# Kernel tuning notes

Measured on AMD Instinct MI355X. Metric: run time of the kernel, lower is better.

## Reference

```python
import jax, jax.numpy as jnp
import numpy as np

H, DH, M, ITERS = 8, 64, 256, 6   # heads, dim_head, num_landmarks, pinv iters
DIM = H * DH                      # 512
KERNEL = 33                       # residual depthwise conv kernel


def setup_inputs() -> dict:
    key = jax.random.key(0)
    ks = jax.random.split(key, 5)
    b, n = 2, 8192                # n multiple of M -> no divisibility padding
    x = jax.random.normal(ks[0], (b, n, DIM), jnp.float32)
    ln_gamma = jnp.ones((DIM,), jnp.float32)
    ln_beta = jnp.zeros((DIM,), jnp.float32)
    w_qkv = jax.random.normal(ks[1], (DIM, 3 * DIM), jnp.float32) * 0.02
    w_out = jax.random.normal(ks[2], (DIM, DIM), jnp.float32) * 0.02
    b_out = jnp.zeros((DIM,), jnp.float32)
    res_kernel = jax.random.normal(ks[3], (H, 1, KERNEL, 1), jnp.float32) * 0.02
    return {"x": x, "ln_gamma": ln_gamma, "ln_beta": ln_beta, "w_qkv": w_qkv,
            "w_out": w_out, "b_out": b_out, "res_kernel": res_kernel}


def _pinv(a, iters):
    # lucidrains moore_penrose_iter_pinv (Newton-Schulz iteration)
    abs_a = jnp.abs(a)
    scale = abs_a.sum(-1).max() * abs_a.sum(-2).max()
    z = jnp.swapaxes(a, -1, -2) / scale
    I = jnp.eye(a.shape[-1], dtype=a.dtype)
    for _ in range(iters):
        az = a @ z
        z = 0.25 * z @ (13.0 * I - az @ (15.0 * I - az @ (7.0 * I - az)))
    return z


def reference(x, ln_gamma, ln_beta, w_qkv, w_out, b_out, res_kernel):
    b, n, d = x.shape
    # pre-LayerNorm (eps 1e-5)
    mu = jnp.mean(x, -1, keepdims=True)
    var = jnp.var(x, -1, keepdims=True)
    xn = (x - mu) * jax.lax.rsqrt(var + 1e-5) * ln_gamma + ln_beta
    # qkv projection (bias-free)
    q, k, v = jnp.split(xn @ w_qkv, 3, axis=-1)
    to_heads = lambda t: t.reshape(b, n, H, DH).transpose(0, 2, 1, 3)  # b h n d
    q, k, v = to_heads(q), to_heads(k), to_heads(v)
    q = q * (DH ** -0.5)
    # landmarks: mean over groups of l consecutive tokens ('(m l) d -> m d')
    l = n // M
    q_l = q.reshape(b, H, M, l, DH).mean(3)  # b h M d
    k_l = k.reshape(b, H, M, l, DH).mean(3)
    sim1 = jnp.einsum('bhnd,bhmd->bhnm', q, k_l)      # queries vs k-landmarks
    sim2 = jnp.einsum('bhid,bhjd->bhij', q_l, k_l)    # landmarks vs landmarks
    sim3 = jnp.einsum('bhmd,bhnd->bhmn', q_l, k)      # q-landmarks vs keys
    a1 = jax.nn.softmax(sim1, axis=-1)
    a2 = jax.nn.softmax(sim2, axis=-1)
    a3 = jax.nn.softmax(sim3, axis=-1)
    a2_inv = _pinv(a2, ITERS)
    out = (a1 @ a2_inv) @ (a3 @ v)  # b h n d
    # residual depthwise conv over the sequence axis (Conv2d kernel (33,1), groups=H)
    pad = KERNEL // 2
    out = out + jax.lax.conv_general_dilated(
        v, res_kernel, (1, 1), [(pad, pad), (0, 0)],
        dimension_numbers=('NCHW', 'OIHW', 'NCHW'), feature_group_count=H)
    out = out.transpose(0, 2, 1, 3).reshape(b, n, d)
    out = out @ w_out + b_out  # to_out Linear (dropout inactive at eval)
    return x + out             # TransLayer residual
```

## Files before the change

kernel.cpp:

```cpp
#include <hip/hip_runtime.h>
#include <math.h>

#define H_ 8
#define DH_ 64
#define DIM_ 512
#define M_ 256
#define N_ 8192
#define BH_ 16
#define LG_ 32
#define KC_ 33
#define CH_ 16
#define NTI_ 8

typedef __attribute__((ext_vector_type(8))) short bf16x8;
typedef __attribute__((ext_vector_type(4))) short s16x4;
typedef __attribute__((ext_vector_type(4))) float f32x4;

__device__ __forceinline__ short f2bf(float f) {
  unsigned u = __float_as_uint(f);
  unsigned r = (u + 0x7FFF + ((u >> 16) & 1)) >> 16;
  return (short)r;
}
__device__ __forceinline__ float bf2f(short s) {
  return __uint_as_float(((unsigned)(unsigned short)s) << 16);
}

__device__ __forceinline__ void mfma_nt_core(const short* __restrict__ A,
                                             const short* __restrict__ Bt, int K,
                                             int m0, int n0, size_t lda, size_t ldb,
                                             f32x4 acc[4][4], short* As, short* Bs) {
  const int tid = threadIdx.x;
  const int wave = tid >> 6, lane = tid & 63;
  const int wr = (wave >> 1) * 64, wc = (wave & 1) * 64;
  const int mi = lane & 15, quad = lane >> 4;
  for (int k0 = 0; k0 < K; k0 += 32) {
#pragma unroll
    for (int t = 0; t < 2; ++t) {
      const int cbase = (t * 4 + wave) * 64;
      const int chunk = cbase + lane;
      const int row = chunk >> 2, cc = (chunk & 3) * 8;
      __builtin_amdgcn_global_load_lds(
          (const __attribute__((address_space(1))) void*)(A + (size_t)(m0 + row) * lda + k0 + cc),
          (__attribute__((address_space(3))) void*)(As + (size_t)cbase * 8), 16, 0, 0);
      __builtin_amdgcn_global_load_lds(
          (const __attribute__((address_space(1))) void*)(Bt + (size_t)(n0 + row) * ldb + k0 + cc),
          (__attribute__((address_space(3))) void*)(Bs + (size_t)cbase * 8), 16, 0, 0);
    }
    __syncthreads();
    bf16x8 af[4], bf[4];
#pragma unroll
    for (int i = 0; i < 4; ++i)
      af[i] = *(const bf16x8*)&As[(wr + i * 16 + mi) * 32 + quad * 8];
#pragma unroll
    for (int j = 0; j < 4; ++j)
      bf[j] = *(const bf16x8*)&Bs[(wc + j * 16 + mi) * 32 + quad * 8];
#pragma unroll
    for (int i = 0; i < 4; ++i)
#pragma unroll
      for (int j = 0; j < 4; ++j)
        acc[i][j] = __builtin_amdgcn_mfma_f32_16x16x32_bf16(af[i], bf[j], acc[i][j], 0, 0, 0);
    __syncthreads();
  }
}

__device__ __forceinline__ void xcd_remap128(int& bx, int& by) {
  const int lin = blockIdx.y * 128 + blockIdx.x;
  const int cpx = (gridDim.y * 128) >> 3;
  const int sw = (lin & 7) * cpx + (lin >> 3);
  bx = sw & 127;
  by = sw >> 7;
}

__global__ __launch_bounds__(256) void qkv_mfma(const short* __restrict__ xnb,
                                                const short* __restrict__ wt,
                                                short* __restrict__ qb, short* __restrict__ kb,
                                                short* __restrict__ vb) {
  __shared__ short As[128 * 32], Bs[128 * 32];
  f32x4 acc[4][4] = {};
  int bx, by;
  xcd_remap128(bx, by);
  const int m0 = bx * 128, n0 = by * 128;
  mfma_nt_core(xnb, wt, DIM_, m0, n0, DIM_, DIM_, acc, As, Bs);
  const int wave = threadIdx.x >> 6, lane = threadIdx.x & 63;
  const int wr = (wave >> 1) * 64, wc = (wave & 1) * 64;
  const int mi = lane & 15, quad = lane >> 4;
  const int which = n0 >> 9;
  short* dst = which == 0 ? qb : which == 1 ? kb : vb;
  const float sc = which == 0 ? 0.125f : 1.0f;
#pragma unroll
  for (int j = 0; j < 4; ++j) {
    const int col = n0 + wc + j * 16 + mi;
    const int h = (col >> 6) & 7, d = col & 63;
#pragma unroll
    for (int i = 0; i < 4; ++i) {
#pragma unroll
      for (int r = 0; r < 4; ++r) {
        const int row = m0 + wr + i * 16 + quad * 4 + r;
        const int b = row >> 13, t = row & (N_ - 1);
        dst[((size_t)(b * H_ + h) * N_ + t) * DH_ + d] = f2bf(acc[i][j][r] * sc);
      }
    }
  }
}

__global__ __launch_bounds__(256) void final_mfma(const short* __restrict__ omb,
                                                  const short* __restrict__ wt,
                                                  const float* __restrict__ x,
                                                  const float* __restrict__ bout,
                                                  float* __restrict__ y) {
  __shared__ short As[128 * 32], Bs[128 * 32];
  f32x4 acc[4][4] = {};
  int bx, by;
  xcd_remap128(bx, by);
  const int m0 = bx * 128, n0 = by * 128;
  mfma_nt_core(omb, wt, DIM_, m0, n0, DIM_, DIM_, acc, As, Bs);
  const int wave = threadIdx.x >> 6, lane = threadIdx.x & 63;
  const int wr = (wave >> 1) * 64, wc = (wave & 1) * 64;
  const int mi = lane & 15, quad = lane >> 4;
#pragma unroll
  for (int j = 0; j < 4; ++j) {
    const int col = n0 + wc + j * 16 + mi;
    const float bo = bout[col];
#pragma unroll
    for (int i = 0; i < 4; ++i) {
#pragma unroll
      for (int r = 0; r < 4; ++r) {
        const int row = m0 + wr + i * 16 + quad * 4 + r;
        y[(size_t)row * DIM_ + col] = acc[i][j][r] + x[(size_t)row * DIM_ + col] + bo;
      }
    }
  }
}

__global__ __launch_bounds__(256) void convt_kernel(const float* __restrict__ in,
                                                    short* __restrict__ out, int K, int N) {
  __shared__ float tile[32][33];
  const int n0 = blockIdx.x * 32, k0 = blockIdx.y * 32;
  const int tx = threadIdx.x & 31, ty = threadIdx.x >> 5;
  for (int r = ty; r < 32; r += 8) tile[r][tx] = in[(size_t)(k0 + r) * N + n0 + tx];
  __syncthreads();
  for (int r = ty; r < 32; r += 8) out[(size_t)(n0 + r) * K + k0 + tx] = f2bf(tile[tx][r]);
}

__global__ __launch_bounds__(256) void vt_kernel(const short* __restrict__ vb,
                                                 short* __restrict__ vtb) {
  __shared__ short tile[32][33];
  const int t0 = blockIdx.x * 32, d0 = blockIdx.y * 32, bh = blockIdx.z;
  const int tx = threadIdx.x & 31, ty = threadIdx.x >> 5;
  for (int r = ty; r < 32; r += 8)
    tile[r][tx] = vb[((size_t)bh * N_ + t0 + r) * DH_ + d0 + tx];
  __syncthreads();
  for (int r = ty; r < 32; r += 8)
    vtb[((size_t)bh * DH_ + d0 + r) * N_ + t0 + tx] = tile[tx][r];
}

__global__ __launch_bounds__(256) void ln_kernel(const float* __restrict__ x,
                                                 const float* __restrict__ gamma,
                                                 const float* __restrict__ beta,
                                                 short* __restrict__ xnb) {
  const int row = blockIdx.x * 4 + (threadIdx.x >> 6);
  const int lane = threadIdx.x & 63;
  const float4* xr = (const float4*)(x + (size_t)row * DIM_) + lane * 2;
  const float4 v0 = xr[0], v1 = xr[1];
  float s = v0.x + v0.y + v0.z + v0.w + v1.x + v1.y + v1.z + v1.w;
  float ss = v0.x * v0.x + v0.y * v0.y + v0.z * v0.z + v0.w * v0.w +
             v1.x * v1.x + v1.y * v1.y + v1.z * v1.z + v1.w * v1.w;
#pragma unroll
  for (int off = 1; off < 64; off <<= 1) {
    s += __shfl_xor(s, off, 64);
    ss += __shfl_xor(ss, off, 64);
  }
  const float mu = s * (1.0f / DIM_);
  const float var = ss * (1.0f / DIM_) - mu * mu;
  const float rs = rsqrtf(var + 1e-5f);
  const float4 g0 = ((const float4*)gamma)[lane * 2], g1 = ((const float4*)gamma)[lane * 2 + 1];
  const float4 b0 = ((const float4*)beta)[lane * 2], b1 = ((const float4*)beta)[lane * 2 + 1];
  bf16x8 o;
  o[0] = f2bf((v0.x - mu) * rs * g0.x + b0.x);
  o[1] = f2bf((v0.y - mu) * rs * g0.y + b0.y);
  o[2] = f2bf((v0.z - mu) * rs * g0.z + b0.z);
  o[3] = f2bf((v0.w - mu) * rs * g0.w + b0.w);
  o[4] = f2bf((v1.x - mu) * rs * g1.x + b1.x);
  o[5] = f2bf((v1.y - mu) * rs * g1.y + b1.y);
  o[6] = f2bf((v1.z - mu) * rs * g1.z + b1.z);
  o[7] = f2bf((v1.w - mu) * rs * g1.w + b1.w);
  *(bf16x8*)(xnb + (size_t)row * DIM_ + lane * 8) = o;
}

__global__ __launch_bounds__(256) void landmark_kernel(const short* __restrict__ qb,
                                                       const short* __restrict__ kb,
                                                       float* __restrict__ ql,
                                                       float* __restrict__ kl,
                                                       short* __restrict__ qlb,
                                                       short* __restrict__ klb) {
  const int idx = blockIdx.x * 256 + threadIdx.x;
  const int d = idx & (DH_ - 1);
  const int m = (idx >> 6) & (M_ - 1);
  const int bh = idx >> 14;
  const size_t base = ((size_t)bh * N_ + m * LG_) * DH_ + d;
  float sq = 0.f, sk = 0.f;
#pragma unroll 8
  for (int t = 0; t < LG_; ++t) {
    sq += bf2f(qb[base + (size_t)t * DH_]);
    sk += bf2f(kb[base + (size_t)t * DH_]);
  }
  sq *= (1.0f / LG_);
  sk *= (1.0f / LG_);
  ql[idx] = sq;
  kl[idx] = sk;
  qlb[idx] = f2bf(sq);
  klb[idx] = f2bf(sk);
}

__global__ __launch_bounds__(256) void sim2_softmax(const float* __restrict__ ql,
                                                    const float* __restrict__ kl,
                                                    float* __restrict__ a2,
                                                    short* __restrict__ a2b) {
  const int i = blockIdx.x, bh = blockIdx.y, j = threadIdx.x;
  __shared__ float qrow[DH_];
  if (j < DH_) qrow[j] = ql[((size_t)bh * M_ + i) * DH_ + j];
  __syncthreads();
  const float* kr = kl + ((size_t)bh * M_ + j) * DH_;
  float s = 0.f;
#pragma unroll 16
  for (int d = 0; d < DH_; ++d) s += qrow[d] * kr[d];
  __shared__ float red[256];
  red[j] = s;
  __syncthreads();
  for (int off = 128; off > 0; off >>= 1) {
    if (j < off) red[j] = fmaxf(red[j], red[j + off]);
    __syncthreads();
  }
  const float mx = red[0];
  __syncthreads();
  const float e = expf(s - mx);
  red[j] = e;
  __syncthreads();
  for (int off = 128; off > 0; off >>= 1) {
    if (j < off) red[j] += red[j + off];
    __syncthreads();
  }
  const float out = e / red[0];
  a2[((size_t)bh * M_ + i) * M_ + j] = out;
  a2b[((size_t)bh * M_ + i) * M_ + j] = f2bf(out);
}

__global__ __launch_bounds__(256) void colmax_kernel(const float* __restrict__ a2,
                                                     unsigned int* __restrict__ scalebits) {
  const int bh = blockIdx.x, j = threadIdx.x;
  const float* mat = a2 + (size_t)bh * M_ * M_;
  float s = 0.f;
  for (int i = 0; i < M_; ++i) s += fabsf(mat[i * M_ + j]);
  __shared__ float red[256];
  red[j] = s;
  __syncthreads();
  for (int off = 128; off > 0; off >>= 1) {
    if (j < off) red[j] = fmaxf(red[j], red[j + off]);
    __syncthreads();
  }
  if (j == 0) atomicMax(scalebits, __float_as_uint(red[0]));
}

__global__ __launch_bounds__(256) void transpose_scale(const float* __restrict__ a2,
                                                       short* __restrict__ z0b,
                                                       const unsigned int* __restrict__ scalebits) {
  const float inv = 1.0f / __uint_as_float(*scalebits);
  const int idx = blockIdx.x * 256 + threadIdx.x;
  const int j = idx & (M_ - 1), i = (idx >> 8) & (M_ - 1), bh = idx >> 16;
  z0b[idx] = f2bf(a2[((size_t)bh * M_ + j) * M_ + i] * inv);
}

__device__ __forceinline__ void ns_core(const short* __restrict__ A, const short* __restrict__ B,
                                        int m0, int n0, short* Bs, f32x4 acc[4]) {
  const int tid = threadIdx.x, wave = tid >> 6, lane = tid & 63;
  const int mi = lane & 15, quad = lane >> 4;
  const int bkk = tid & 31, g = tid >> 5;
  bf16x8 bv[8];
#pragma unroll
  for (int kc = 0; kc < 8; ++kc)
    bv[kc] = *(const bf16x8*)(B + (size_t)(kc * 32 + bkk) * M_ + n0 + g * 8);
  const short* arow = A + (size_t)(m0 + wave * 16 + mi) * M_;
  bf16x8 af[8];
#pragma unroll
  for (int k0 = 0; k0 < 8; ++k0)
    af[k0] = *(const bf16x8*)(arow + k0 * 32 + quad * 8);
#pragma unroll
  for (int kc = 0; kc < 8; ++kc)
#pragma unroll
    for (int e = 0; e < 8; ++e)
      Bs[(g * 8 + e) * 260 + kc * 32 + bkk] = bv[kc][e];
  __syncthreads();
#pragma unroll
  for (int k0 = 0; k0 < 8; ++k0) {
#pragma unroll
    for (int j = 0; j < 4; ++j) {
      union { bf16x8 v; s16x4 h[2]; } bfr;
      const short* bp = &Bs[(j * 16 + mi) * 260 + k0 * 32 + quad * 8];
      bfr.h[0] = *(const s16x4*)bp;
      bfr.h[1] = *(const s16x4*)(bp + 4);
      acc[j] = __builtin_amdgcn_mfma_f32_16x16x32_bf16(af[k0], bfr.v, acc[j], 0, 0, 0);
    }
  }
}

__device__ __forceinline__ int ns_remap() {
  const int lin = blockIdx.y * 16 + blockIdx.x;
  return (lin & 7) * (gridDim.y << 1) + (lin >> 3);
}

__global__ __launch_bounds__(256) void ns_gemm0(const short* __restrict__ A,
                                                const short* __restrict__ B,
                                                short* __restrict__ C) {
  __shared__ short Bs[64 * 260];
  const int id = ns_remap();
  const int bx = id & 15, by = id >> 4;
  const int m0 = (bx >> 2) * 64, n0 = (bx & 3) * 64;
  const size_t mo = (size_t)by * (M_ * M_);
  f32x4 acc[4] = {};
  ns_core(A + mo, B + mo, m0, n0, Bs, acc);
  const int wave = threadIdx.x >> 6, lane = threadIdx.x & 63;
  const int mi = lane & 15, quad = lane >> 4;
#pragma unroll
  for (int j = 0; j < 4; ++j)
#pragma unroll
    for (int r = 0; r < 4; ++r) {
      const int row = m0 + wave * 16 + quad * 4 + r, col = n0 + j * 16 + mi;
      C[mo + (size_t)row * M_ + col] = f2bf(acc[j][r]);
    }
}

__global__ __launch_bounds__(256) void ns_stageA(const short* __restrict__ z,
                                                 const short* __restrict__ y,
                                                 short* __restrict__ p1,
                                                 short* __restrict__ y2,
                                                 short* __restrict__ w) {
  __shared__ short Bs[64 * 260];
  const int id = ns_remap();
  const int bx = id & 15, by = id >> 4;
  const int m0 = (bx >> 2) * 64, n0 = (bx & 3) * 64;
  const int sel = by & 1;
  const size_t mo = (size_t)(by >> 1) * (M_ * M_);
  f32x4 acc[4] = {};
  ns_core((sel ? y : z) + mo, y + mo, m0, n0, Bs, acc);
  const int wave = threadIdx.x >> 6, lane = threadIdx.x & 63;
  const int mi = lane & 15, quad = lane >> 4;
#pragma unroll
  for (int j = 0; j < 4; ++j)
#pragma unroll
    for (int r = 0; r < 4; ++r) {
      const int row = m0 + wave * 16 + quad * 4 + r, col = n0 + j * 16 + mi;
      const size_t idx = mo + (size_t)row * M_ + col;
      if (sel) {
        y2[idx] = f2bf(acc[j][r]);
        w[idx] = f2bf(1.75f * bf2f(y[idx]) - 0.25f * acc[j][r]);
      } else {
        p1[idx] = f2bf(acc[j][r]);
      }
    }
}

__global__ __launch_bounds__(256) void ns_stageB(const short* __restrict__ p1,
                                                 const short* __restrict__ y2,
                                                 const short* __restrict__ w,
                                                 const short* __restrict__ z,
                                                 const short* __restrict__ y,
                                                 short* __restrict__ zo,
                                                 short* __restrict__ yo,
                                                 float* __restrict__ zf, int zonly) {
  __shared__ short Bs[64 * 260];
  const int id = ns_remap();
  const int bx = id & 15, by = id >> 4;
  const int m0 = (bx >> 2) * 64, n0 = (bx & 3) * 64;
  const int sel = zonly ? 0 : (by & 1);
  const size_t mo = (size_t)(zonly ? by : (by >> 1)) * (M_ * M_);
  f32x4 acc[4] = {};
  ns_core((sel ? y2 : p1) + mo, w + mo, m0, n0, Bs, acc);
  const int wave = threadIdx.x >> 6, lane = threadIdx.x & 63;
  const int mi = lane & 15, quad = lane >> 4;
#pragma unroll
  for (int j = 0; j < 4; ++j)
#pragma unroll
    for (int r = 0; r < 4; ++r) {
      const int row = m0 + wave * 16 + quad * 4 + r, col = n0 + j * 16 + mi;
      const size_t idx = mo + (size_t)row * M_ + col;
      if (sel) {
        yo[idx] = f2bf(3.25f * bf2f(y[idx]) - 3.75f * bf2f(y2[idx]) + acc[j][r]);
      } else {
        const float v = 3.25f * bf2f(z[idx]) - 3.75f * bf2f(p1[idx]) + acc[j][r];
        zo[idx] = f2bf(v);
        if (zf) zf[idx] = v;
      }
    }
}

__device__ __forceinline__ void mm_step(float (*As)[68], float (*Bs)[68],
                                        int tr, int tc, float acc[4][4]) {
#pragma unroll
  for (int kk = 0; kk < 16; ++kk) {
    const float4 a4 = *(const float4*)&As[kk][tr * 4];
    const float4 b4 = *(const float4*)&Bs[kk][tc * 4];
    const float a[4] = {a4.x, a4.y, a4.z, a4.w};
    const float b[4] = {b4.x, b4.y, b4.z, b4.w};
#pragma unroll
    for (int i = 0; i < 4; ++i)
#pragma unroll
      for (int j = 0; j < 4; ++j) acc[i][j] = fmaf(a[i], b[j], acc[i][j]);
  }
}

__device__ __forceinline__ void load_a_tile(const float* A, int lda, int m0, int k0,
                                            int tid, float (*As)[68]) {
  const int r = tid >> 2, kq = tid & 3;
  const float4 a4 = *(const float4*)(A + (size_t)(m0 + r) * lda + k0 + kq * 4);
  As[kq * 4 + 0][r] = a4.x;
  As[kq * 4 + 1][r] = a4.y;
  As[kq * 4 + 2][r] = a4.z;
  As[kq * 4 + 3][r] = a4.w;
}

__device__ __forceinline__ void load_b_nn(const float* B, int ldb, int k0, int n0,
                                          int tid, float (*Bs)[68]) {
  const int kr = tid >> 4, c4 = tid & 15;
  const float4 b4 = *(const float4*)(B + (size_t)(k0 + kr) * ldb + n0 + c4 * 4);
  *(float4*)&Bs[kr][c4 * 4] = b4;
}

__global__ __launch_bounds__(256) void gemm_nn64(const float* __restrict__ A, int lda,
                                                 long long strideA,
                                                 const float* __restrict__ B, long long strideB,
                                                 float* __restrict__ C, long long strideC,
                                                 int kchunk) {
  const int bz = blockIdx.z;
  A += (size_t)bz * strideA;
  B += (size_t)bz * strideB;
  C += (size_t)bz * strideC;
  const int m0 = blockIdx.x * 64;
  const int tid = threadIdx.x, tr = tid >> 4, tc = tid & 15;
  __shared__ float As[16][68], Bs[16][68];
  float acc[4][4] = {};
  for (int k0 = 0; k0 < kchunk; k0 += 16) {
    load_a_tile(A, lda, m0, k0, tid, As);
    load_b_nn(B, DH_, k0, 0, tid, Bs);
    __syncthreads();
    mm_step(As, Bs, tr, tc, acc);
    __syncthreads();
  }
#pragma unroll
  for (int i = 0; i < 4; ++i) {
    const int row = m0 + tr * 4 + i;
    *(float4*)(C + (size_t)row * DH_ + tc * 4) =
        make_float4(acc[i][0], acc[i][1], acc[i][2], acc[i][3]);
  }
}

__device__ __forceinline__ void stage_ks(const short* __restrict__ kb, int bh, int n0,
                                         int wave, int lane, short* ks) {
#pragma unroll
  for (int i = 0; i < 2; ++i) {
    const int cb = i * 256 + wave * 64;
    const int c = cb + lane;
    const int row = c >> 3, cc = c & 7;
    __builtin_amdgcn_global_load_lds(
        (const __attribute__((address_space(1))) void*)(
            kb + ((size_t)bh * N_ + n0 + row) * DH_ + ((cc ^ (row & 7)) * 8)),
        (__attribute__((address_space(3))) void*)(ks + (size_t)cb * 8), 16, 0, 0);
  }
}

__device__ __forceinline__ void stage_vs(const short* __restrict__ vtb, int bh, int n0,
                                         int wave, int lane, short* vs) {
#pragma unroll
  for (int i = 0; i < 2; ++i) {
    const int cb = i * 256 + wave * 64;
    const int c = cb + lane;
    const int row = c >> 3, cc = c & 7;
    __builtin_amdgcn_global_load_lds(
        (const __attribute__((address_space(1))) void*)(
            vtb + ((size_t)bh * DH_ + row) * N_ + n0 + ((cc ^ (row & 7)) * 8)),
        (__attribute__((address_space(3))) void*)(vs + (size_t)cb * 8), 16, 0, 0);
  }
}

__global__ __launch_bounds__(256) void a3_flash(const short* __restrict__ qlb,
                                                const short* __restrict__ kb,
                                                const short* __restrict__ vtb,
                                                float* __restrict__ Opart,
                                                float* __restrict__ mpart,
                                                float* __restrict__ lpart) {
  const int chunk = blockIdx.x, rt = blockIdx.y, bh = blockIdx.z;
  __shared__ short ks[2][64 * 64];
  __shared__ short vs[2][64 * 64];
  __shared__ short ps[64 * 64];
  const int tid = threadIdx.x, wave = tid >> 6, lane = tid & 63;
  const int mi = lane & 15, quad = lane >> 4;
  const short* qrow = qlb + ((size_t)bh * M_ + rt * 64 + wave * 16 + mi) * DH_;
  const bf16x8 aq0 = *(const bf16x8*)(qrow + quad * 8);
  const bf16x8 aq1 = *(const bf16x8*)(qrow + 32 + quad * 8);
  float m[4] = {-INFINITY, -INFINITY, -INFINITY, -INFINITY};
  float l[4] = {0.f, 0.f, 0.f, 0.f};
  f32x4 o[4] = {};
  const int nbase = chunk * (N_ / CH_);
  stage_ks(kb, bh, nbase, wave, lane, ks[0]);
  stage_vs(vtb, bh, nbase, wave, lane, vs[0]);
  __syncthreads();
  for (int t = 0; t < NTI_; ++t) {
    const int cur = t & 1;
    if (t + 1 < NTI_) {
      stage_ks(kb, bh, nbase + (t + 1) * 64, wave, lane, ks[cur ^ 1]);
      stage_vs(vtb, bh, nbase + (t + 1) * 64, wave, lane, vs[cur ^ 1]);
    }
    f32x4 s[4];
#pragma unroll
    for (int j = 0; j < 4; ++j) {
      const int row = j * 16 + mi;
      const bf16x8 b0 = *(const bf16x8*)&ks[cur][row * 64 + ((quad ^ (row & 7)) * 8)];
      const bf16x8 b1 = *(const bf16x8*)&ks[cur][row * 64 + (((quad + 4) ^ (row & 7)) * 8)];
      f32x4 z = {0.f, 0.f, 0.f, 0.f};
      z = __builtin_amdgcn_mfma_f32_16x16x32_bf16(aq0, b0, z, 0, 0, 0);
      s[j] = __builtin_amdgcn_mfma_f32_16x16x32_bf16(aq1, b1, z, 0, 0, 0);
    }
    float alpha[4];
#pragma unroll
    for (int r = 0; r < 4; ++r) {
      float v = fmaxf(fmaxf(s[0][r], s[1][r]), fmaxf(s[2][r], s[3][r]));
      v = fmaxf(v, __shfl_xor(v, 1, 64));
      v = fmaxf(v, __shfl_xor(v, 2, 64));
      v = fmaxf(v, __shfl_xor(v, 4, 64));
      v = fmaxf(v, __shfl_xor(v, 8, 64));
      const float mnew = fmaxf(m[r], v);
      alpha[r] = __expf(m[r] - mnew);
      m[r] = mnew;
    }
    float rs[4] = {0.f, 0.f, 0.f, 0.f};
#pragma unroll
    for (int j = 0; j < 4; ++j)
#pragma unroll
      for (int r = 0; r < 4; ++r) {
        const float p = __expf(s[j][r] - m[r]);
        rs[r] += p;
        const int prow = wave * 16 + quad * 4 + r;
        const int pcol = j * 16 + mi;
        ps[prow * 64 + (((pcol >> 3) ^ (prow & 7)) * 8) + (pcol & 7)] = f2bf(p);
      }
#pragma unroll
    for (int r = 0; r < 4; ++r) {
      l[r] = l[r] * alpha[r] + rs[r];
#pragma unroll
      for (int j = 0; j < 4; ++j) o[j][r] *= alpha[r];
    }
    const int prow = wave * 16 + mi;
    const bf16x8 ap0 = *(const bf16x8*)&ps[prow * 64 + ((quad ^ (mi & 7)) * 8)];
    const bf16x8 ap1 = *(const bf16x8*)&ps[prow * 64 + (((quad + 4) ^ (mi & 7)) * 8)];
#pragma unroll
    for (int j = 0; j < 4; ++j) {
      const int vrow = j * 16 + mi;
      const bf16x8 b0 = *(const bf16x8*)&vs[cur][vrow * 64 + ((quad ^ (vrow & 7)) * 8)];
      const bf16x8 b1 = *(const bf16x8*)&vs[cur][vrow * 64 + (((quad + 4) ^ (vrow & 7)) * 8)];
      o[j] = __builtin_amdgcn_mfma_f32_16x16x32_bf16(ap0, b0, o[j], 0, 0, 0);
      o[j] = __builtin_amdgcn_mfma_f32_16x16x32_bf16(ap1, b1, o[j], 0, 0, 0);
    }
    __syncthreads();
  }
#pragma unroll
  for (int r = 0; r < 4; ++r) {
    float v = l[r];
    v += __shfl_xor(v, 1, 64);
    v += __shfl_xor(v, 2, 64);
    v += __shfl_xor(v, 4, 64);
    v += __shfl_xor(v, 8, 64);
    l[r] = v;
  }
  const int p2 = bh * 4 + rt;
  float* Ob = Opart + ((size_t)chunk * 64 + p2) * 4096;
#pragma unroll
  for (int j = 0; j < 4; ++j)
#pragma unroll
    for (int r = 0; r < 4; ++r)
      Ob[(wave * 16 + quad * 4 + r) * 64 + j * 16 + mi] = o[j][r];
  if (mi == 0) {
#pragma unroll
    for (int r = 0; r < 4; ++r) {
      mpart[((size_t)chunk * 64 + p2) * 64 + wave * 16 + quad * 4 + r] = m[r];
      lpart[((size_t)chunk * 64 + p2) * 64 + wave * 16 + quad * 4 + r] = l[r];
    }
  }
}

__global__ __launch_bounds__(256) void a3_combine(const float* __restrict__ Opart,
                                                  const float* __restrict__ mpart,
                                                  const float* __restrict__ lpart,
                                                  float* __restrict__ a3v) {
  const int p2 = blockIdx.x, ds = blockIdx.y;
  const int bh = p2 >> 2, rt = p2 & 3;
  __shared__ float wgt[CH_][64];
  const int tid = threadIdx.x;
  if (tid < 64) {
    float mg = -INFINITY;
#pragma unroll
    for (int c = 0; c < CH_; ++c) mg = fmaxf(mg, mpart[((size_t)c * 64 + p2) * 64 + tid]);
    float e[CH_], lg = 0.f;
#pragma unroll
    for (int c = 0; c < CH_; ++c) {
      e[c] = __expf(mpart[((size_t)c * 64 + p2) * 64 + tid] - mg);
      lg += lpart[((size_t)c * 64 + p2) * 64 + tid] * e[c];
    }
    const float inv = 1.f / lg;
#pragma unroll
    for (int c = 0; c < CH_; ++c) wgt[c][tid] = e[c] * inv;
  }
  __syncthreads();
  for (int i = ds * 1024 + tid; i < ds * 1024 + 1024; i += 256) {
    const int row = i >> 6, d = i & 63;
    float s = 0.f;
#pragma unroll
    for (int c = 0; c < CH_; ++c) s += Opart[((size_t)c * 64 + p2) * 4096 + i] * wgt[c][row];
    a3v[((size_t)bh * M_ + rt * 64 + row) * DH_ + d] = s;
  }
}

__global__ __launch_bounds__(256) void w2t_kernel(const float* __restrict__ w2,
                                                  short* __restrict__ w2tb) {
  const int bh = blockIdx.x, tid = threadIdx.x;
  for (int i = tid; i < M_ * DH_; i += 256) {
    const int r = i >> 6, d = i & 63;
    w2tb[((size_t)bh * DH_ + d) * M_ + r] = f2bf(w2[(size_t)bh * M_ * DH_ + i]);
  }
}

__global__ __launch_bounds__(256, 4) void a1_conv(const short* __restrict__ qb,
                                                  const short* __restrict__ klb,
                                                  const short* __restrict__ w2tb,
                                                  const short* __restrict__ vtb,
                                                  const float* __restrict__ rk,
                                                  short* __restrict__ omb) {
  __shared__ __align__(16) char smem[34944];
  short* kls = (short*)smem;
  short* ps = (short*)smem;
  short* vwin = (short*)(smem + 17920);
  short* band = (short*)(smem + 32768);
  const int bh = blockIdx.y, t0 = blockIdx.x * 64;
  const int b = bh >> 3, h = bh & 7;
  const int tid = threadIdx.x, wave = tid >> 6, lane = tid & 63;
  const int mi = lane & 15, quad = lane >> 4;

  const short* qrow = qb + ((size_t)bh * N_ + t0 + wave * 16 + mi) * DH_;
  const bf16x8 aq0 = *(const bf16x8*)(qrow + quad * 8);
  const bf16x8 aq1 = *(const bf16x8*)(qrow + 32 + quad * 8);

  const int vd = tid & 63, cg0 = tid >> 6;
  bf16x8 vreg[4];
  {
    const short* vrow = vtb + ((size_t)bh * DH_ + vd) * N_;
#pragma unroll
    for (int slot = 0; slot < 4; ++slot) {
      const int ch = cg0 + slot * 4;
      bf16x8 vv = {};
      if (ch < 14) {
        const int tbase = t0 - 16 + ch * 8;
        if (tbase >= 0 && tbase + 8 <= N_) {
          vv = *(const bf16x8*)(vrow + tbase);
        } else {
#pragma unroll
          for (int e = 0; e < 8; ++e) {
            const int tt = tbase + e;
            vv[e] = (tt >= 0 && tt < N_) ? vrow[tt] : (short)0;
          }
        }
      }
      vreg[slot] = vv;
    }
  }
#pragma unroll
  for (int i = 0; i < 4; ++i) {
    const int idx = tid + i * 256;
    const int r = idx >> 6, c = idx & 63, u = c - r;
    band[r * 68 + c] = (u >= 0 && u < KC_) ? f2bf(rk[h * KC_ + u]) : (short)0;
  }

#pragma unroll
  for (int i = 0; i < 8; ++i) {
    const int cb = i * 256 + wave * 64;
    const int c = cb + lane;
    const int row = c >> 3, cc = c & 7;
    __builtin_amdgcn_global_load_lds(
        (const __attribute__((address_space(1))) void*)(
            klb + ((size_t)bh * M_ + row) * DH_ + (cc ^ (row & 7)) * 8),
        (__attribute__((address_space(3))) void*)(kls + (size_t)cb * 8), 16, 0, 0);
  }
  __syncthreads();

  f32x4 s[16] = {};
#pragma unroll
  for (int f = 0; f < 16; ++f) {
    const int row = f * 16 + mi;
    const bf16x8 blo = *(const bf16x8*)&kls[row * 64 + ((quad ^ (row & 7)) * 8)];
    const bf16x8 bhi = *(const bf16x8*)&kls[row * 64 + (((quad + 4) ^ (row & 7)) * 8)];
    f32x4 z = __builtin_amdgcn_mfma_f32_16x16x32_bf16(aq0, blo, s[f], 0, 0, 0);
    s[f] = __builtin_amdgcn_mfma_f32_16x16x32_bf16(aq1, bhi, z, 0, 0, 0);
  }
  float lsum[4];
#pragma unroll
  for (int r = 0; r < 4; ++r) {
    float v = s[0][r];
#pragma unroll
    for (int f = 1; f < 16; ++f) v = fmaxf(v, s[f][r]);
    v = fmaxf(v, __shfl_xor(v, 1, 64));
    v = fmaxf(v, __shfl_xor(v, 2, 64));
    v = fmaxf(v, __shfl_xor(v, 4, 64));
    v = fmaxf(v, __shfl_xor(v, 8, 64));
    float sum = 0.f;
#pragma unroll
    for (int f = 0; f < 16; ++f) {
      const float p = __expf(s[f][r] - v);
      s[f][r] = p;
      sum += p;
    }
    lsum[r] = sum;
  }
  __syncthreads();

#pragma unroll
  for (int slot = 0; slot < 4; ++slot) {
    const int ch = cg0 + slot * 4;
    if (ch < 14) *(bf16x8*)&vwin[vd * 116 + ch * 8] = vreg[slot];
  }

  f32x4 o[4] = {};
#pragma unroll
  for (int half = 0; half < 2; ++half) {
#pragma unroll
    for (int f = 0; f < 8; ++f)
#pragma unroll
      for (int r = 0; r < 4; ++r)
        ps[(wave * 16 + quad * 4 + r) * 140 + f * 16 + mi] = f2bf(s[half * 8 + f][r]);
#pragma unroll
    for (int k0 = 0; k0 < 4; ++k0) {
      union { bf16x8 v; s16x4 hh[2]; } ap;
      const short* pp = &ps[(wave * 16 + mi) * 140 + k0 * 32 + quad * 8];
      ap.hh[0] = *(const s16x4*)pp;
      ap.hh[1] = *(const s16x4*)(pp + 4);
#pragma unroll
      for (int j = 0; j < 4; ++j) {
        const bf16x8 bw = *(const bf16x8*)(w2tb + ((size_t)bh * DH_ + j * 16 + mi) * M_ +
                                           (half * 4 + k0) * 32 + quad * 8);
        o[j] = __builtin_amdgcn_mfma_f32_16x16x32_bf16(ap.v, bw, o[j], 0, 0, 0);
      }
    }
  }
#pragma unroll
  for (int r = 0; r < 4; ++r) {
    float v = lsum[r];
    v += __shfl_xor(v, 1, 64);
    v += __shfl_xor(v, 2, 64);
    v += __shfl_xor(v, 4, 64);
    v += __shfl_xor(v, 8, 64);
    const float inv = 1.f / v;
#pragma unroll
    for (int j = 0; j < 4; ++j) o[j][r] *= inv;
  }
  __syncthreads();

#pragma unroll
  for (int ks = 0; ks < 2; ++ks) {
    union { bf16x8 v; s16x4 hh[2]; } ab;
    const short* bp = &band[mi * 68 + ks * 32 + quad * 8];
    ab.hh[0] = *(const s16x4*)bp;
    ab.hh[1] = *(const s16x4*)(bp + 4);
#pragma unroll
    for (int j = 0; j < 4; ++j) {
      union { bf16x8 v; s16x4 hh[2]; } bv;
      const short* vp = &vwin[(j * 16 + mi) * 116 + wave * 16 + ks * 32 + quad * 8];
      bv.hh[0] = *(const s16x4*)vp;
      bv.hh[1] = *(const s16x4*)(vp + 4);
      o[j] = __builtin_amdgcn_mfma_f32_16x16x32_bf16(ab.v, bv.v, o[j], 0, 0, 0);
    }
  }
#pragma unroll
  for (int j = 0; j < 4; ++j) {
    const int d = j * 16 + mi;
#pragma unroll
    for (int r = 0; r < 4; ++r) {
      const int t = t0 + wave * 16 + quad * 4 + r;
      omb[((size_t)(b * N_ + t)) * DIM_ + h * DH_ + d] = f2bf(o[j][r]);
    }
  }
}

extern "C" void kernel_launch(void* const* d_in, const int* in_sizes, int n_in,
                              void* d_out, int out_size, void* d_ws, size_t ws_size,
                              hipStream_t stream) {
  (void)in_sizes; (void)n_in; (void)out_size;
  const float* x = (const float*)d_in[0];
  const float* gamma = (const float*)d_in[1];
  const float* beta = (const float*)d_in[2];
  const float* wqkv = (const float*)d_in[3];
  const float* wout = (const float*)d_in[4];
  const float* bout = (const float*)d_in[5];
  const float* rk = (const float*)d_in[6];
  float* y = (float*)d_out;
  float* ws = (float*)d_ws;

  size_t o = 0;
  short* xnb = (short*)(ws + o);   o += (size_t)2 * N_ * DIM_ / 2;
  short* wqkvt = (short*)(ws + o); o += (size_t)3 * DIM_ * DIM_ / 2;
  short* woutt = (short*)(ws + o); o += (size_t)DIM_ * DIM_ / 2;
  short* qb = (short*)(ws + o);    o += (size_t)BH_ * N_ * DH_ / 2;
  short* kb = (short*)(ws + o);    o += (size_t)BH_ * N_ * DH_ / 2;
  short* vb = (short*)(ws + o);    o += (size_t)BH_ * N_ * DH_ / 2;
  short* vtb = (short*)(ws + o);   o += (size_t)BH_ * N_ * DH_ / 2;
  float* ql = ws + o;  o += (size_t)BH_ * M_ * DH_;
  float* kl = ws + o;  o += (size_t)BH_ * M_ * DH_;
  short* qlb = (short*)(ws + o); o += (size_t)BH_ * M_ * DH_ / 2;
  short* klb = (short*)(ws + o); o += (size_t)BH_ * M_ * DH_ / 2;
  float* a2 = ws + o;  o += (size_t)BH_ * M_ * M_;
  float* z0f = ws + o; o += (size_t)BH_ * M_ * M_;
  short* a2b = (short*)(ws + o); o += (size_t)BH_ * M_ * M_ / 2;
  short* zb0 = (short*)(ws + o); o += (size_t)BH_ * M_ * M_ / 2;
  short* zb1 = (short*)(ws + o); o += (size_t)BH_ * M_ * M_ / 2;
  short* yb0 = (short*)(ws + o); o += (size_t)BH_ * M_ * M_ / 2;
  short* yb1 = (short*)(ws + o); o += (size_t)BH_ * M_ * M_ / 2;
  short* p1b = (short*)(ws + o); o += (size_t)BH_ * M_ * M_ / 2;
  short* y2b = (short*)(ws + o); o += (size_t)BH_ * M_ * M_ / 2;
  short* wb  = (short*)(ws + o); o += (size_t)BH_ * M_ * M_ / 2;
  float* Opart = ws + o; o += (size_t)CH_ * 64 * 4096;
  float* mpart = ws + o; o += (size_t)CH_ * 64 * 64;
  float* lpart = ws + o; o += (size_t)CH_ * 64 * 64;
  float* a3v = ws + o; o += (size_t)BH_ * M_ * DH_;
  float* w2 = ws + o;  o += (size_t)BH_ * M_ * DH_;
  short* w2tb = (short*)(ws + o); o += (size_t)BH_ * M_ * DH_ / 2;
  short* omb = (short*)(ws + o);  o += (size_t)2 * N_ * DIM_ / 2;
  unsigned int* scalebits = (unsigned int*)(ws + o); o += 16;
  if (ws_size < o * sizeof(float)) return;

  (void)hipMemsetAsync(scalebits, 0, 64, stream);
  ln_kernel<<<2 * N_ / 4, 256, 0, stream>>>(x, gamma, beta, xnb);
  convt_kernel<<<dim3(3 * DIM_ / 32, DIM_ / 32), 256, 0, stream>>>(wqkv, wqkvt, DIM_, 3 * DIM_);
  convt_kernel<<<dim3(DIM_ / 32, DIM_ / 32), 256, 0, stream>>>(wout, woutt, DIM_, DIM_);
  qkv_mfma<<<dim3(2 * N_ / 128, 3 * DIM_ / 128), 256, 0, stream>>>(xnb, wqkvt, qb, kb, vb);
  vt_kernel<<<dim3(N_ / 32, 2, BH_), 256, 0, stream>>>(vb, vtb);

  landmark_kernel<<<BH_ * M_ * DH_ / 256, 256, 0, stream>>>(qb, kb, ql, kl, qlb, klb);
  sim2_softmax<<<dim3(M_, BH_), 256, 0, stream>>>(ql, kl, a2, a2b);
  colmax_kernel<<<BH_, 256, 0, stream>>>(a2, scalebits);
  transpose_scale<<<BH_ * M_ * M_ / 256, 256, 0, stream>>>(a2, zb0, scalebits);

  a3_flash<<<dim3(CH_, 4, BH_), 256, 0, stream>>>(qlb, kb, vtb, Opart, mpart, lpart);
  a3_combine<<<dim3(64, 4), 256, 0, stream>>>(Opart, mpart, lpart, a3v);

  ns_gemm0<<<dim3(16, BH_), 256, 0, stream>>>(a2b, zb0, yb0);
  short* zc = zb0; short* zn = zb1; short* yc = yb0; short* yn = yb1;
  for (int it = 0; it < 6; ++it) {
    const int last = (it == 5);
    ns_stageA<<<dim3(16, 2 * BH_), 256, 0, stream>>>(zc, yc, p1b, y2b, wb);
    ns_stageB<<<dim3(16, last ? BH_ : 2 * BH_), 256, 0, stream>>>(
        p1b, y2b, wb, zc, yc, zn, yn, last ? z0f : nullptr, last);
    short* t;
    t = zc; zc = zn; zn = t;
    t = yc; yc = yn; yn = t;
  }

  gemm_nn64<<<dim3(M_ / 64, 1, BH_), 256, 0, stream>>>(
      z0f, M_, (long long)M_ * M_, a3v, (long long)M_ * DH_, w2, (long long)M_ * DH_, M_);
  w2t_kernel<<<BH_, 256, 0, stream>>>(w2, w2tb);

  a1_conv<<<dim3(N_ / 64, BH_), 256, 0, stream>>>(qb, klb, w2tb, vtb, rk, omb);

  final_mfma<<<dim3(2 * N_ / 128, DIM_ / 128), 256, 0, stream>>>(omb, woutt, x, bout, y);
}
```

Measured before the change: 453.8 us.

## Fuse Newton-Schulz pinv iterations into one cooperative kernel with grid syncs

Replaces the 13 separate Newton-Schulz GEMM launches with a single cooperative kernel of 512 blocks that uses grid.sync between stages, which removes per-launch overhead and the gaps between launches. It also fuses the bf16 transpose of w2 into the gemm_nn64 epilogue, so the w2t_kernel launch and the fp32 w2 buffer are no longer needed. The XCD block remapping is dropped from the qkv and final GEMMs. Grid-wide barriers add their own sync cost, need all 512 blocks to be co-resident, and the new transposed stores in gemm_nn64 are strided.

New measurement: 1.764 ms. +288.8%, slower.

```diff
diff --git a/kernel.cpp b/kernel.cpp
--- a/kernel.cpp
+++ b/kernel.cpp
@@ -1,5 +1,8 @@
 #include <hip/hip_runtime.h>
+#include <hip/hip_cooperative_groups.h>
 #include <math.h>
+
+namespace cg = cooperative_groups;
 
 #define H_ 8
 #define DH_ 64
@@ -63,23 +66,13 @@
   }
 }
 
-__device__ __forceinline__ void xcd_remap128(int& bx, int& by) {
-  const int lin = blockIdx.y * 128 + blockIdx.x;
-  const int cpx = (gridDim.y * 128) >> 3;
-  const int sw = (lin & 7) * cpx + (lin >> 3);
-  bx = sw & 127;
-  by = sw >> 7;
-}
-
 __global__ __launch_bounds__(256) void qkv_mfma(const short* __restrict__ xnb,
                                                 const short* __restrict__ wt,
                                                 short* __restrict__ qb, short* __restrict__ kb,
                                                 short* __restrict__ vb) {
   __shared__ short As[128 * 32], Bs[128 * 32];
   f32x4 acc[4][4] = {};
-  int bx, by;
-  xcd_remap128(bx, by);
-  const int m0 = bx * 128, n0 = by * 128;
+  const int m0 = blockIdx.x * 128, n0 = blockIdx.y * 128;
   mfma_nt_core(xnb, wt, DIM_, m0, n0, DIM_, DIM_, acc, As, Bs);
   const int wave = threadIdx.x >> 6, lane = threadIdx.x & 63;
   const int wr = (wave >> 1) * 64, wc = (wave & 1) * 64;
@@ -110,9 +103,7 @@
                                                   float* __restrict__ y) {
   __shared__ short As[128 * 32], Bs[128 * 32];
   f32x4 acc[4][4] = {};
-  int bx, by;
-  xcd_remap128(bx, by);
-  const int m0 = bx * 128, n0 = by * 128;
+  const int m0 = blockIdx.x * 128, n0 = blockIdx.y * 128;
   mfma_nt_core(omb, wt, DIM_, m0, n0, DIM_, DIM_, acc, As, Bs);
   const int wave = threadIdx.x >> 6, lane = threadIdx.x & 63;
   const int wr = (wave >> 1) * 64, wc = (wave & 1) * 64;
@@ -303,94 +294,112 @@
   }
 }
 
-__device__ __forceinline__ int ns_remap() {
-  const int lin = blockIdx.y * 16 + blockIdx.x;
-  return (lin & 7) * (gridDim.y << 1) + (lin >> 3);
-}
-
-__global__ __launch_bounds__(256) void ns_gemm0(const short* __restrict__ A,
-                                                const short* __restrict__ B,
-                                                short* __restrict__ C) {
+__device__ __forceinline__ int ns_swz(int bid, int n) {
+  return (bid & 7) * (n >> 3) + (bid >> 3);
+}
+
+__global__ __launch_bounds__(256) void ns_fused(const short* __restrict__ a2b,
+                                                short* __restrict__ zb0, short* __restrict__ zb1,
+                                                short* __restrict__ yb0, short* __restrict__ yb1,
+                                                short* __restrict__ p1b, short* __restrict__ y2b,
+                                                short* __restrict__ wb,
+                                                float* __restrict__ z0f) {
+  cg::grid_group grid = cg::this_grid();
   __shared__ short Bs[64 * 260];
-  const int id = ns_remap();
-  const int bx = id & 15, by = id >> 4;
-  const int m0 = (bx >> 2) * 64, n0 = (bx & 3) * 64;
-  const size_t mo = (size_t)by * (M_ * M_);
-  f32x4 acc[4] = {};
-  ns_core(A + mo, B + mo, m0, n0, Bs, acc);
+  const int bid = blockIdx.x;
   const int wave = threadIdx.x >> 6, lane = threadIdx.x & 63;
   const int mi = lane & 15, quad = lane >> 4;
-#pragma unroll
-  for (int j = 0; j < 4; ++j)
-#pragma unroll
-    for (int r = 0; r < 4; ++r) {
-      const int row = m0 + wave * 16 + quad * 4 + r, col = n0 + j * 16 + mi;
-      C[mo + (size_t)row * M_ + col] = f2bf(acc[j][r]);
-    }
-}
-
-__global__ __launch_bounds__(256) void ns_stageA(const short* __restrict__ z,
-                                                 const short* __restrict__ y,
-                                                 short* __restrict__ p1,
-                                                 short* __restrict__ y2,
-                                                 short* __restrict__ w) {
-  __shared__ short Bs[64 * 260];
-  const int id = ns_remap();
-  const int bx = id & 15, by = id >> 4;
-  const int m0 = (bx >> 2) * 64, n0 = (bx & 3) * 64;
-  const int sel = by & 1;
-  const size_t mo = (size_t)(by >> 1) * (M_ * M_);
-  f32x4 acc[4] = {};
-  ns_core((sel ? y : z) + mo, y + mo, m0, n0, Bs, acc);
-  const int wave = threadIdx.x >> 6, lane = threadIdx.x & 63;
-  const int mi = lane & 15, quad = lane >> 4;
-#pragma unroll
-  for (int j = 0; j < 4; ++j)
-#pragma unroll
-    for (int r = 0; r < 4; ++r) {
-      const int row = m0 + wave * 16 + quad * 4 + r, col = n0 + j * 16 + mi;
-      const size_t idx = mo + (size_t)row * M_ + col;
-      if (sel) {
-        y2[idx] = f2bf(acc[j][r]);
-        w[idx] = f2bf(1.75f * bf2f(y[idx]) - 0.25f * acc[j][r]);
-      } else {
-        p1[idx] = f2bf(acc[j][r]);
+
+  if (bid < 256) {
+    const int w = ns_swz(bid, 256);
+    const int bx = w & 15, bh = w >> 4;
+    const int m0 = (bx >> 2) * 64, n0 = (bx & 3) * 64;
+    const size_t mo = (size_t)bh * (M_ * M_);
+    f32x4 acc[4] = {};
+    ns_core(a2b + mo, zb0 + mo, m0, n0, Bs, acc);
+#pragma unroll
+    for (int j = 0; j < 4; ++j)
+#pragma unroll
+      for (int r = 0; r < 4; ++r) {
+        const int row = m0 + wave * 16 + quad * 4 + r, col = n0 + j * 16 + mi;
+        yb0[mo + (size_t)row * M_ + col] = f2bf(acc[j][r]);
       }
-    }
-}
-
-__global__ __launch_bounds__(256) void ns_stageB(const short* __restrict__ p1,
-                                                 const short* __restrict__ y2,
-                                                 const short* __restrict__ w,
-                                                 const short* __restrict__ z,
-                                                 const short* __restrict__ y,
-                                                 short* __restrict__ zo,
-                                                 short* __restrict__ yo,
-                                                 float* __restrict__ zf, int zonly) {
-  __shared__ short Bs[64 * 260];
-  const int id = ns_remap();
-  const int bx = id & 15, by = id >> 4;
-  const int m0 = (bx >> 2) * 64, n0 = (bx & 3) * 64;
-  const int sel = zonly ? 0 : (by & 1);
-  const size_t mo = (size_t)(zonly ? by : (by >> 1)) * (M_ * M_);
-  f32x4 acc[4] = {};
-  ns_core((sel ? y2 : p1) + mo, w + mo, m0, n0, Bs, acc);
-  const int wave = threadIdx.x >> 6, lane = threadIdx.x & 63;
-  const int mi = lane & 15, quad = lane >> 4;
-#pragma unroll
-  for (int j = 0; j < 4; ++j)
-#pragma unroll
-    for (int r = 0; r < 4; ++r) {
-      const int row = m0 + wave * 16 + quad * 4 + r, col = n0 + j * 16 + mi;
-      const size_t idx = mo + (size_t)row * M_ + col;
-      if (sel) {
-        yo[idx] = f2bf(3.25f * bf2f(y[idx]) - 3.75f * bf2f(y2[idx]) + acc[j][r]);
-      } else {
-        const float v = 3.25f * bf2f(z[idx]) - 3.75f * bf2f(p1[idx]) + acc[j][r];
-        zo[idx] = f2bf(v);
-        if (zf) zf[idx] = v;
-      }
-    }
+  }
+  __threadfence();
+  grid.sync();
+
+  for (int it = 0; it < 6; ++it) {
+    const short* zc = (it & 1) ? zb1 : zb0;
+    const short* yc = (it & 1) ? yb1 : yb0;
+    short* zn = (it & 1) ? zb0 : zb1;
+    const int last = (it == 5);
+
+    {
+      const int w = ns_swz(bid, 512);
+      const int bx = w & 15, by = w >> 4;
+      const int m0 = (bx >> 2) * 64, n0 = (bx & 3) * 64;
+      const int sel = by & 1;
+      const size_t mo = (size_t)(by >> 1) * (M_ * M_);
+      f32x4 acc[4] = {};
+      ns_core((sel ? yc : zc) + mo, yc + mo, m0, n0, Bs, acc);
+#pragma unroll
+      for (int j = 0; j < 4; ++j)
+#pragma unroll
+        for (int r = 0; r < 4; ++r) {
+          const int row = m0 + wave * 16 + quad * 4 + r, col = n0 + j * 16 + mi;
+          const size_t idx = mo + (size_t)row * M_ + col;
+          if (sel) {
+            y2b[idx] = f2bf(acc[j][r]);
+            wb[idx] = f2bf(1.75f * bf2f(yc[idx]) - 0.25f * acc[j][r]);
+          } else {
+            p1b[idx] = f2bf(acc[j][r]);
+          }
+        }
+    }
+    __threadfence();
+    grid.sync();
+
+    if (!last) {
+      short* yn = (it & 1) ? yb0 : yb1;
+      const int w = ns_swz(bid, 512);
+      const int bx = w & 15, by = w >> 4;
+      const int m0 = (bx >> 2) * 64, n0 = (bx & 3) * 64;
+      const int sel = by & 1;
+      const size_t mo = (size_t)(by >> 1) * (M_ * M_);
+      f32x4 acc[4] = {};
+      ns_core((sel ? y2b : p1b) + mo, wb + mo, m0, n0, Bs, acc);
+#pragma unroll
+      for (int j = 0; j < 4; ++j)
+#pragma unroll
+        for (int r = 0; r < 4; ++r) {
+          const int row = m0 + wave * 16 + quad * 4 + r, col = n0 + j * 16 + mi;
+          const size_t idx = mo + (size_t)row * M_ + col;
+          if (sel) {
+            yn[idx] = f2bf(3.25f * bf2f(yc[idx]) - 3.75f * bf2f(y2b[idx]) + acc[j][r]);
+          } else {
+            zn[idx] = f2bf(3.25f * bf2f(zc[idx]) - 3.75f * bf2f(p1b[idx]) + acc[j][r]);
+          }
+        }
+      __threadfence();
+      grid.sync();
+    } else if (bid < 256) {
+      const int w = ns_swz(bid, 256);
+      const int bx = w & 15, bh = w >> 4;
+      const int m0 = (bx >> 2) * 64, n0 = (bx & 3) * 64;
+      const size_t mo = (size_t)bh * (M_ * M_);
+      f32x4 acc[4] = {};
+      ns_core(p1b + mo, wb + mo, m0, n0, Bs, acc);
+#pragma unroll
+      for (int j = 0; j < 4; ++j)
+#pragma unroll
+        for (int r = 0; r < 4; ++r) {
+          const int row = m0 + wave * 16 + quad * 4 + r, col = n0 + j * 16 + mi;
+          const size_t idx = mo + (size_t)row * M_ + col;
+          const float v = 3.25f * bf2f(zc[idx]) - 3.75f * bf2f(p1b[idx]) + acc[j][r];
+          z0f[idx] = v;
+        }
+    }
+  }
 }
 
 __device__ __forceinline__ void mm_step(float (*As)[68], float (*Bs)[68],
@@ -428,12 +437,10 @@
 __global__ __launch_bounds__(256) void gemm_nn64(const float* __restrict__ A, int lda,
                                                  long long strideA,
                                                  const float* __restrict__ B, long long strideB,
-                                                 float* __restrict__ C, long long strideC,
-                                                 int kchunk) {
+                                                 short* __restrict__ w2tb, int kchunk) {
   const int bz = blockIdx.z;
   A += (size_t)bz * strideA;
   B += (size_t)bz * strideB;
-  C += (size_t)bz * strideC;
   const int m0 = blockIdx.x * 64;
   const int tid = threadIdx.x, tr = tid >> 4, tc = tid & 15;
   __shared__ float As[16][68], Bs[16][68];
@@ -448,8 +455,9 @@
 #pragma unroll
   for (int i = 0; i < 4; ++i) {
     const int row = m0 + tr * 4 + i;
-    *(float4*)(C + (size_t)row * DH_ + tc * 4) =
-        make_float4(acc[i][0], acc[i][1], acc[i][2], acc[i][3]);
+#pragma unroll
+    for (int j = 0; j < 4; ++j)
+      w2tb[((size_t)bz * DH_ + tc * 4 + j) * M_ + row] = f2bf(acc[i][j]);
   }
 }
 
@@ -615,15 +623,6 @@
 #pragma unroll
     for (int c = 0; c < CH_; ++c) s += Opart[((size_t)c * 64 + p2) * 4096 + i] * wgt[c][row];
     a3v[((size_t)bh * M_ + rt * 64 + row) * DH_ + d] = s;
-  }
-}
-
-__global__ __launch_bounds__(256) void w2t_kernel(const float* __restrict__ w2,
-                                                  short* __restrict__ w2tb) {
-  const int bh = blockIdx.x, tid = threadIdx.x;
-  for (int i = tid; i < M_ * DH_; i += 256) {
-    const int r = i >> 6, d = i & 63;
-    w2tb[((size_t)bh * DH_ + d) * M_ + r] = f2bf(w2[(size_t)bh * M_ * DH_ + i]);
   }
 }
 
@@ -826,7 +825,6 @@
   float* mpart = ws + o; o += (size_t)CH_ * 64 * 64;
   float* lpart = ws + o; o += (size_t)CH_ * 64 * 64;
   float* a3v = ws + o; o += (size_t)BH_ * M_ * DH_;
-  float* w2 = ws + o;  o += (size_t)BH_ * M_ * DH_;
   short* w2tb = (short*)(ws + o); o += (size_t)BH_ * M_ * DH_ / 2;
   short* omb = (short*)(ws + o);  o += (size_t)2 * N_ * DIM_ / 2;
   unsigned int* scalebits = (unsigned int*)(ws + o); o += 16;
@@ -847,21 +845,14 @@
   a3_flash<<<dim3(CH_, 4, BH_), 256, 0, stream>>>(qlb, kb, vtb, Opart, mpart, lpart);
   a3_combine<<<dim3(64, 4), 256, 0, stream>>>(Opart, mpart, lpart, a3v);
 
-  ns_gemm0<<<dim3(16, BH_), 256, 0, stream>>>(a2b, zb0, yb0);
-  short* zc = zb0; short* zn = zb1; short* yc = yb0; short* yn = yb1;
-  for (int it = 0; it < 6; ++it) {
-    const int last = (it == 5);
-    ns_stageA<<<dim3(16, 2 * BH_), 256, 0, stream>>>(zc, yc, p1b, y2b, wb);
-    ns_stageB<<<dim3(16, last ? BH_ : 2 * BH_), 256, 0, stream>>>(
-        p1b, y2b, wb, zc, yc, zn, yn, last ? z0f : nullptr, last);
-    short* t;
-    t = zc; zc = zn; zn = t;
-    t = yc; yc = yn; yn = t;
+  {
+    void* nsArgs[] = {(void*)&a2b, (void*)&zb0, (void*)&zb1, (void*)&yb0, (void*)&yb1,
+                      (void*)&p1b, (void*)&y2b, (void*)&wb, (void*)&z0f};
+    (void)hipLaunchCooperativeKernel((void*)ns_fused, dim3(512), dim3(256), nsArgs, 0, stream);
   }
 
   gemm_nn64<<<dim3(M_ / 64, 1, BH_), 256, 0, stream>>>(
-      z0f, M_, (long long)M_ * M_, a3v, (long long)M_ * DH_, w2, (long long)M_ * DH_, M_);
-  w2t_kernel<<<BH_, 256, 0, stream>>>(w2, w2tb);
+      z0f, M_, (long long)M_ * M_, a3v, (long long)M_ * DH_, w2tb, M_);
 
   a1_conv<<<dim3(N_ / 64, BH_), 256, 0, stream>>>(qb, klb, w2tb, vtb, rk, omb);
 
```
